# Optimization experiments

Measured on AMD Instinct MI355X. Metric: run time of the kernel, lower is better.

Reference implementation:

```python
import jax, jax.numpy as jnp
import numpy as np

VP, B, C, H, W = 8, 2, 512, 16, 16
N_HEAD = 8


def setup_inputs() -> dict:
    key = jax.random.key(0)
    k0, k1, k2, k3, k4 = jax.random.split(key, 5)
    x = jax.random.normal(k0, (VP, B, C, H, W), dtype=jnp.float32)
    s = 1.0 / np.sqrt(C)
    Wqkv = jax.random.normal(k1, (C, 3 * C), dtype=jnp.float32) * s
    bqkv = jnp.zeros((3 * C,), dtype=jnp.float32)
    Wo = jax.random.normal(k2, (C, C), dtype=jnp.float32) * s
    bo = jnp.zeros((C,), dtype=jnp.float32)
    return {"x": x, "Wqkv": Wqkv, "bqkv": bqkv, "Wo": Wo, "bo": bo}


def reference(x, Wqkv, bqkv, Wo, bo):
    vp, b, c, h, w = x.shape
    hw = h * w
    T = vp * hw
    hd = c // N_HEAD
    # 'v b c h w -> b (v h w) c'
    xs = jnp.transpose(x, (1, 0, 3, 4, 2)).reshape(b, T, c)
    qkv = xs @ Wqkv + bqkv  # [b, T, 3c]
    q, k, v = jnp.split(qkv, 3, axis=-1)
    def heads(t):
        return jnp.transpose(t.reshape(b, T, N_HEAD, hd), (0, 2, 1, 3))  # [b, nh, T, hd]
    q, k, v = heads(q), heads(k), heads(v)
    scale = 1.0 / np.sqrt(hd)
    att = jnp.einsum('bhqd,bhkd->bhqk', q, k) * scale  # [b, nh, T, T]
    # block-causal mask: token in block i attends to all tokens in blocks 0..i
    blk = jnp.arange(T) // hw
    allowed = blk[None, :] <= blk[:, None]  # [T, T]
    att = jnp.where(allowed, att, -jnp.inf)
    att = jax.nn.softmax(att, axis=-1)
    y = jnp.einsum('bhqk,bhkd->bhqd', att, v)  # [b, nh, T, hd]
    y = jnp.transpose(y, (0, 2, 1, 3)).reshape(b, T, c)
    y = y @ Wo + bo
    # 'b (v h w) c -> v b c h w'
    y = jnp.transpose(y.reshape(b, vp, h, w, c), (1, 0, 4, 2, 3))
    return y
```

## Files before the change

kernel.cpp:

```cpp
#include <hip/hip_runtime.h>
#include <hip/hip_bf16.h>
#include <stdint.h>

#define VPn 8
#define BBn 2
#define CCn 512
#define NHn 8
#define HDn 64
#define Tn  2048
#define Mn  4096
#define N1n 1536
#define Kn  512
#define QSC 0.180336880111120425f

typedef __attribute__((ext_vector_type(8))) short bf16x8;
typedef __attribute__((ext_vector_type(4))) short s16x4;
typedef __attribute__((ext_vector_type(4))) float f32x4;
typedef __attribute__((ext_vector_type(16))) float f32x16;
typedef unsigned short u16;
typedef unsigned int   u32;

__device__ __forceinline__ u16 f2bf(float f) {
  return __builtin_bit_cast(u16, __float2bfloat16(f));
}
__device__ __forceinline__ void gload16(const void* g, void* l) {
  __builtin_amdgcn_global_load_lds(
      (const __attribute__((address_space(1))) u32*)g,
      (__attribute__((address_space(3))) u32*)l, 16, 0, 0);
}

__global__ __launch_bounds__(256) void conv_x(const float* __restrict__ x, u16* __restrict__ A) {
  int bi = blockIdx.x;
  int vb = bi >> 5;
  int ct = (bi >> 2) & 7;
  int ht = bi & 3;
  int v = vb >> 1, b = vb & 1;
  __shared__ float t[64][65];
  int tid = threadIdx.x, col = tid & 63, r4 = tid >> 6;
  const float* src = x + ((size_t)vb * CCn + ct * 64) * 256 + ht * 64;
#pragma unroll
  for (int i = 0; i < 16; ++i) {
    int row = i * 4 + r4;
    t[row][col] = src[row * 256 + col];
  }
  __syncthreads();
  u16* dst = A + ((size_t)(b * Tn + v * 256 + ht * 64)) * Kn + ct * 64;
#pragma unroll
  for (int i = 0; i < 16; ++i) {
    int row = i * 4 + r4;
    dst[row * Kn + col] = f2bf(t[col][row]);
  }
}

__global__ __launch_bounds__(256) void convw(const float* __restrict__ Win, u16* __restrict__ Wt,
                                             int R, int Cc) {
  int tpr = Cc >> 6;
  int rt = blockIdx.x / tpr, ct = blockIdx.x % tpr;
  __shared__ float t[64][65];
  int tid = threadIdx.x, col = tid & 63, r4 = tid >> 6;
  const float* src = Win + (size_t)(rt * 64) * Cc + ct * 64;
#pragma unroll
  for (int i = 0; i < 16; ++i) {
    int row = i * 4 + r4;
    t[row][col] = src[row * Cc + col];
  }
  __syncthreads();
  u16* dst = Wt + (size_t)(ct * 64) * R + rt * 64;
#pragma unroll
  for (int i = 0; i < 16; ++i) {
    int row = i * 4 + r4;
    dst[row * R + col] = f2bf(t[col][row]);
  }
}


__global__ __launch_bounds__(256, 2) void gemm_qkv(
    const u16* __restrict__ A, const u16* __restrict__ Bt, const float* __restrict__ bias,
    u16* __restrict__ Qo, u16* __restrict__ Kp, u16* __restrict__ Vp) {
  const int nt = N1n / 128;
  int m0 = (blockIdx.x / nt) * 64;
  int n0 = (blockIdx.x % nt) * 128;
  __shared__ __align__(16) u16 As[64 * 64];
  __shared__ __align__(16) u16 Bs[128 * 64];
  int tid = threadIdx.x, lane = tid & 63, w = tid >> 6;
  int wr = w & 1, wc = w >> 1;
  int li = lane & 15, g = lane >> 4;
  int rsub = lane >> 3, slot = lane & 7;
  int srcslot = slot ^ rsub;
  f32x4 acc[2][4] = {};
  for (int k0 = 0; k0 < Kn; k0 += 64) {
    __syncthreads();
#pragma unroll
    for (int i = 0; i < 2; ++i) {
      int ci = w * 2 + i;
      int row = ci * 8 + rsub;
      gload16(A + (size_t)(m0 + row) * Kn + k0 + srcslot * 8, (char*)As + ci * 1024);
    }
#pragma unroll
    for (int i = 0; i < 4; ++i) {
      int ci = w * 4 + i;
      int row = ci * 8 + rsub;
      gload16(Bt + (size_t)(n0 + row) * Kn + k0 + srcslot * 8, (char*)Bs + ci * 1024);
    }
    __syncthreads();
#pragma unroll
    for (int kk = 0; kk < 2; ++kk) {
      bf16x8 af[2], bfr[4];
#pragma unroll
      for (int mi = 0; mi < 2; ++mi) {
        int row = wr * 32 + mi * 16 + li;
        int sw = ((kk * 4 + g) ^ (row & 7)) * 8;
        af[mi] = *(const bf16x8*)(As + row * 64 + sw);
      }
#pragma unroll
      for (int ni = 0; ni < 4; ++ni) {
        int row = wc * 64 + ni * 16 + li;
        int sw = ((kk * 4 + g) ^ (row & 7)) * 8;
        bfr[ni] = *(const bf16x8*)(Bs + row * 64 + sw);
      }
#pragma unroll
      for (int mi = 0; mi < 2; ++mi)
#pragma unroll
        for (int ni = 0; ni < 4; ++ni)
          acc[mi][ni] = __builtin_amdgcn_mfma_f32_16x16x32_bf16(af[mi], bfr[ni], acc[mi][ni], 0, 0, 0);
    }
  }
#pragma unroll
  for (int ni = 0; ni < 4; ++ni) {
    int n = n0 + wc * 64 + ni * 16 + li;
    float bn = bias[n];
    int sel = n >> 9, c = n & 511, hh = c >> 6, d = c & 63;
    if (sel == 0) {
#pragma unroll
      for (int mi = 0; mi < 2; ++mi) {
#pragma unroll
        for (int r = 0; r < 4; ++r) {
          int m = m0 + wr * 32 + mi * 16 + g * 4 + r;
          int bq = m >> 11, t = m & 2047;
          Qo[((size_t)((bq * NHn + hh) * Tn + t)) * HDn + d] = f2bf((acc[mi][ni][r] + bn) * QSC);
        }
      }
    } else if (sel == 1) {
      int kc = d >> 4, khi = (d >> 3) & 1, kj = d & 7;
#pragma unroll
      for (int mi = 0; mi < 2; ++mi) {
#pragma unroll
        for (int r = 0; r < 4; ++r) {
          int m = m0 + wr * 32 + mi * 16 + g * 4 + r;
          int bq = m >> 11, t = m & 2047;
          size_t off = (size_t)(bq * NHn + hh) * 131072 + (size_t)(t >> 5) * 2048 +
                       kc * 512 + khi * 256 + (t & 31) * 8 + kj;
          Kp[off] = f2bf(acc[mi][ni][r] + bn);
        }
      }
    } else {
      int dh = d >> 5, lqd = d & 31;
#pragma unroll
      for (int mi = 0; mi < 2; ++mi) {
        int mb = m0 + wr * 32 + mi * 16 + g * 4;
        int bq = mb >> 11, t0 = mb & 2047;
        size_t off = (size_t)(bq * NHn + hh) * 131072 + (size_t)(t0 >> 5) * 2048 +
                     dh * 1024 + ((t0 >> 4) & 1) * 512 + lqd * 16 +
                     ((t0 >> 2) & 1) * 8 + ((t0 >> 3) & 1) * 4;
        s16x4 ov;
#pragma unroll
        for (int r = 0; r < 4; ++r) ov[r] = (short)f2bf(acc[mi][ni][r] + bn);
        *(s16x4*)(Vp + off) = ov;
      }
    }
  }
}

__global__ __launch_bounds__(256, 4) void attn(
    const u16* __restrict__ Q, const u16* __restrict__ Kp, const u16* __restrict__ Vp,
    u16* __restrict__ Y) {
  int idx = blockIdx.x;
  int bh = (idx & 7) | (((idx >> 3) & 1) << 3);
  int qt = 63 - (idx >> 4);
  int b = bh >> 3, h = bh & 7;
  int qrow0 = qt << 5;
  int nkeys = ((qt >> 3) + 1) << 8;
  int qtr = nkeys >> 2;
  int tid = threadIdx.x;
  int w = tid >> 6;
  int kbeg = w * qtr, kend = kbeg + qtr;
  int lane = tid & 63;
  int lq = lane & 31;
  int hi = lane >> 5;

  const u16* Qb = Q + ((size_t)(bh * Tn + qrow0)) * HDn;
  const u16* Kb = Kp + (size_t)bh * 131072;
  const u16* Vb = Vp + (size_t)bh * 131072;
  int kof = hi * 256 + lq * 8;
  int vof = lq * 16 + hi * 8;

  bf16x8 qf[4];
  {
    const u16* qp = Qb + (size_t)lq * HDn + hi * 8;
#pragma unroll
    for (int c = 0; c < 4; ++c) qf[c] = *(const bf16x8*)(qp + c * 16);
  }

  float mrun = -1e30f, lrun = 0.f;
  f32x16 oacc0 = {}, oacc1 = {};

  bf16x8 kc[4];
#pragma unroll
  for (int c = 0; c < 4; ++c)
    kc[c] = *(const bf16x8*)(Kb + (size_t)(kbeg >> 5) * 2048 + c * 512 + kof);

  for (int k0 = kbeg; k0 < kend; k0 += 32) {
    int kt = k0 >> 5;
    int ktn = (k0 + 32 < kend) ? (kt + 1) : kt;
    bf16x8 knf[4];
#pragma unroll
    for (int c = 0; c < 4; ++c)
      knf[c] = *(const bf16x8*)(Kb + (size_t)ktn * 2048 + c * 512 + kof);
    const u16* vt = Vb + (size_t)kt * 2048 + vof;
    bf16x8 va0 = *(const bf16x8*)(vt);
    bf16x8 vb0 = *(const bf16x8*)(vt + 512);
    bf16x8 va1 = *(const bf16x8*)(vt + 1024);
    bf16x8 vb1 = *(const bf16x8*)(vt + 1536);

    f32x16 s = {};
    __builtin_amdgcn_s_setprio(1);
#pragma unroll
    for (int c = 0; c < 4; ++c)
      s = __builtin_amdgcn_mfma_f32_32x32x16_bf16(kc[c], qf[c], s, 0, 0, 0);
    __builtin_amdgcn_s_setprio(0);

    float m0 = fmaxf(fmaxf(fmaxf(fmaxf(s[0], s[1]), fmaxf(s[2], s[3])),
                           fmaxf(fmaxf(s[4], s[5]), fmaxf(s[6], s[7]))),
                     fmaxf(fmaxf(fmaxf(s[8], s[9]), fmaxf(s[10], s[11])),
                           fmaxf(fmaxf(s[12], s[13]), fmaxf(s[14], s[15]))));
    float mall = fmaxf(m0, __shfl_xor(m0, 32));
    if (!__all(mall <= mrun + 8.0f)) {
      float mnew = fmaxf(mrun, mall);
      float fc = exp2f(mrun - mnew);
      mrun = mnew;
      lrun *= fc;
#pragma unroll
      for (int j = 0; j < 16; ++j) { oacc0[j] *= fc; oacc1[j] *= fc; }
    }
    float p[16];
#pragma unroll
    for (int j = 0; j < 16; ++j) p[j] = exp2f(s[j] - mrun);
    lrun += (((p[0] + p[1]) + (p[2] + p[3])) + ((p[4] + p[5]) + (p[6] + p[7]))) +
            (((p[8] + p[9]) + (p[10] + p[11])) + ((p[12] + p[13]) + (p[14] + p[15])));

    u32 cw[8];
#pragma unroll
    for (int a = 0; a < 8; ++a)
      cw[a] = (u32)f2bf(p[2 * a]) | ((u32)f2bf(p[2 * a + 1]) << 16);
    bf16x8 pfA, pfB;
    {
      __attribute__((ext_vector_type(4))) int pa = {(int)cw[0], (int)cw[1], (int)cw[2], (int)cw[3]};
      __attribute__((ext_vector_type(4))) int pb = {(int)cw[4], (int)cw[5], (int)cw[6], (int)cw[7]};
      pfA = __builtin_bit_cast(bf16x8, pa);
      pfB = __builtin_bit_cast(bf16x8, pb);
    }

    __builtin_amdgcn_s_setprio(1);
    oacc0 = __builtin_amdgcn_mfma_f32_32x32x16_bf16(va0, pfA, oacc0, 0, 0, 0);
    oacc0 = __builtin_amdgcn_mfma_f32_32x32x16_bf16(vb0, pfB, oacc0, 0, 0, 0);
    oacc1 = __builtin_amdgcn_mfma_f32_32x32x16_bf16(va1, pfA, oacc1, 0, 0, 0);
    oacc1 = __builtin_amdgcn_mfma_f32_32x32x16_bf16(vb1, pfB, oacc1, 0, 0, 0);
    __builtin_amdgcn_s_setprio(0);
#pragma unroll
    for (int c = 0; c < 4; ++c) kc[c] = knf[c];
  }

  lrun += __shfl_xor(lrun, 32);

  __shared__ float Ol[4][32][68];
  __shared__ float ml[2][4][32];
  {
    float* op = &Ol[w][lq][hi * 4];
#pragma unroll
    for (int a = 0; a < 4; ++a) {
      f32x4 v0 = {oacc0[4 * a], oacc0[4 * a + 1], oacc0[4 * a + 2], oacc0[4 * a + 3]};
      f32x4 v1 = {oacc1[4 * a], oacc1[4 * a + 1], oacc1[4 * a + 2], oacc1[4 * a + 3]};
      *(f32x4*)(op + a * 8) = v0;
      *(f32x4*)(op + 32 + a * 8) = v1;
    }
    if (lane < 32) { ml[0][w][lq] = mrun; ml[1][w][lq] = lrun; }
  }
  __syncthreads();

#pragma unroll
  for (int task = tid; task < 512; task += 256) {
    int q = task >> 4, quad = task & 15;
    float m0v = ml[0][0][q], m1v = ml[0][1][q], m2v = ml[0][2][q], m3v = ml[0][3][q];
    float mx = fmaxf(fmaxf(m0v, m1v), fmaxf(m2v, m3v));
    float w0 = exp2f(m0v - mx), w1 = exp2f(m1v - mx);
    float w2 = exp2f(m2v - mx), w3 = exp2f(m3v - mx);
    float l = ml[1][0][q] * w0 + ml[1][1][q] * w1 + ml[1][2][q] * w2 + ml[1][3][q] * w3;
    float inv = 1.0f / l;
    f32x4 o0 = *(const f32x4*)&Ol[0][q][quad * 4];
    f32x4 o1 = *(const f32x4*)&Ol[1][q][quad * 4];
    f32x4 o2 = *(const f32x4*)&Ol[2][q][quad * 4];
    f32x4 o3 = *(const f32x4*)&Ol[3][q][quad * 4];
    s16x4 y;
#pragma unroll
    for (int r = 0; r < 4; ++r)
      y[r] = (short)f2bf((o0[r] * w0 + o1[r] * w1 + o2[r] * w2 + o3[r] * w3) * inv);
    *(s16x4*)(Y + ((size_t)(b * Tn + qrow0 + q)) * CCn + h * HDn + quad * 4) = y;
  }
}

__global__ __launch_bounds__(256, 2) void gemm_out(
    const u16* __restrict__ A, const u16* __restrict__ Bt, const float* __restrict__ bias,
    float* __restrict__ Y2) {
  const int nt = 4;
  int m0 = (blockIdx.x / nt) * 64;
  int n0 = (blockIdx.x % nt) * 128;
  __shared__ __align__(16) u16 As[64 * 64];
  __shared__ __align__(16) u16 Bs[128 * 64];
  int tid = threadIdx.x, lane = tid & 63, w = tid >> 6;
  int wr = w & 1, wc = w >> 1;
  int li = lane & 15, g = lane >> 4;
  int rsub = lane >> 3, slot = lane & 7;
  int srcslot = slot ^ rsub;
  f32x4 acc[2][4] = {};
  for (int k0 = 0; k0 < Kn; k0 += 64) {
    __syncthreads();
#pragma unroll
    for (int i = 0; i < 2; ++i) {
      int ci = w * 2 + i;
      int row = ci * 8 + rsub;
      gload16(A + (size_t)(m0 + row) * Kn + k0 + srcslot * 8, (char*)As + ci * 1024);
    }
#pragma unroll
    for (int i = 0; i < 4; ++i) {
      int ci = w * 4 + i;
      int row = ci * 8 + rsub;
      gload16(Bt + (size_t)(n0 + row) * Kn + k0 + srcslot * 8, (char*)Bs + ci * 1024);
    }
    __syncthreads();
#pragma unroll
    for (int kk = 0; kk < 2; ++kk) {
      bf16x8 af[2], bfr[4];
#pragma unroll
      for (int mi = 0; mi < 2; ++mi) {
        int row = wr * 32 + mi * 16 + li;
        int sw = ((kk * 4 + g) ^ (row & 7)) * 8;
        af[mi] = *(const bf16x8*)(As + row * 64 + sw);
      }
#pragma unroll
      for (int ni = 0; ni < 4; ++ni) {
        int row = wc * 64 + ni * 16 + li;
        int sw = ((kk * 4 + g) ^ (row & 7)) * 8;
        bfr[ni] = *(const bf16x8*)(Bs + row * 64 + sw);
      }
#pragma unroll
      for (int mi = 0; mi < 2; ++mi)
#pragma unroll
        for (int ni = 0; ni < 4; ++ni)
          acc[mi][ni] = __builtin_amdgcn_mfma_f32_16x16x32_bf16(af[mi], bfr[ni], acc[mi][ni], 0, 0, 0);
    }
  }
#pragma unroll
  for (int ni = 0; ni < 4; ++ni) {
    int n = n0 + wc * 64 + ni * 16 + li;
    float bn = bias[n];
#pragma unroll
    for (int mi = 0; mi < 2; ++mi) {
#pragma unroll
      for (int r = 0; r < 4; ++r) {
        int m = m0 + wr * 32 + mi * 16 + g * 4 + r;
        Y2[(size_t)m * CCn + n] = acc[mi][ni][r] + bn;
      }
    }
  }
}

__global__ __launch_bounds__(256) void otrans(const float* __restrict__ Y2, float* __restrict__ out) {
  int bi = blockIdx.x;
  int vb = bi >> 5;
  int ht = (bi >> 3) & 3;
  int ct = bi & 7;
  int v = vb >> 1, b = vb & 1;
  __shared__ float t[64][65];
  int tid = threadIdx.x, col = tid & 63, r4 = tid >> 6;
  const float* src = Y2 + (size_t)(b * Tn + v * 256 + ht * 64) * CCn + ct * 64;
#pragma unroll
  for (int i = 0; i < 16; ++i) {
    int row = i * 4 + r4;
    t[row][col] = src[(size_t)row * CCn + col];
  }
  __syncthreads();
  float* dst = out + ((size_t)vb * CCn + ct * 64) * 256 + ht * 64;
#pragma unroll
  for (int i = 0; i < 16; ++i) {
    int row = i * 4 + r4;
    dst[(size_t)row * 256 + col] = t[col][row];
  }
}

extern "C" void kernel_launch(void* const* d_in, const int* in_sizes, int n_in,
                              void* d_out, int out_size, void* d_ws, size_t ws_size,
                              hipStream_t stream) {
  (void)in_sizes; (void)n_in; (void)out_size; (void)ws_size;
  const float* x    = (const float*)d_in[0];
  const float* Wqkv = (const float*)d_in[1];
  const float* bqkv = (const float*)d_in[2];
  const float* Wo   = (const float*)d_in[3];
  const float* bo   = (const float*)d_in[4];
  float* out = (float*)d_out;
  char* ws = (char*)d_ws;
  const size_t MB = 1ull << 20;
  u16*   Abf   = (u16*)(ws + 0);
  u16*   WqkvT = (u16*)(ws + 4 * MB);
  u16*   WoT   = (u16*)(ws + 5 * MB + 512 * 1024);
  u16*   Qb    = (u16*)(ws + 6 * MB);
  u16*   Kb    = (u16*)(ws + 10 * MB);
  u16*   VTb   = (u16*)(ws + 14 * MB);
  float* Y2    = (float*)(ws + 6 * MB);

  conv_x<<<512, 256, 0, stream>>>(x, Abf);
  convw<<<192, 256, 0, stream>>>(Wqkv, WqkvT, Kn, N1n);
  convw<<<64, 256, 0, stream>>>(Wo, WoT, Kn, CCn);
  gemm_qkv<<<64 * 12, 256, 0, stream>>>(Abf, WqkvT, bqkv, Qb, Kb, VTb);
  attn<<<1024, 256, 0, stream>>>(Qb, Kb, VTb, Abf);
  gemm_out<<<64 * 4, 256, 0, stream>>>(Abf, WoT, bo, Y2);
  otrans<<<512, 256, 0, stream>>>(Y2, out);
}
```

Baseline: 71.90 us.

## Fuse output transpose into out-projection GEMM and use packed bf16 converts

Removes the separate otrans kernel and the Y2 fp32 intermediate by having gemm_out write directly in the v b c h w layout with f32x4 stores along hw. The out GEMM tile shrinks to 64x64 to double the block count, with occupancy raised to 4. The scalar bf16 conversions in the attention P packing, the V store and the Y store are replaced by the v_cvt_pk_bf16_f32 inline asm. The trade-offs are less B-tile reuse per block and strided output stores across channels.

Measured after the change: 62.22 us. 1.16x faster.

```diff
diff --git a/kernel.cpp b/kernel.cpp
--- a/kernel.cpp
+++ b/kernel.cpp
@@ -17,11 +17,17 @@
 typedef __attribute__((ext_vector_type(4))) short s16x4;
 typedef __attribute__((ext_vector_type(4))) float f32x4;
 typedef __attribute__((ext_vector_type(16))) float f32x16;
+typedef __attribute__((ext_vector_type(2))) unsigned int u32x2;
 typedef unsigned short u16;
 typedef unsigned int   u32;
 
 __device__ __forceinline__ u16 f2bf(float f) {
   return __builtin_bit_cast(u16, __float2bfloat16(f));
+}
+__device__ __forceinline__ u32 cvtpk(float lo, float hi) {
+  u32 r;
+  asm("v_cvt_pk_bf16_f32 %0, %1, %2" : "=v"(r) : "v"(lo), "v"(hi));
+  return r;
 }
 __device__ __forceinline__ void gload16(const void* g, void* l) {
   __builtin_amdgcn_global_load_lds(
@@ -162,10 +168,10 @@
         size_t off = (size_t)(bq * NHn + hh) * 131072 + (size_t)(t0 >> 5) * 2048 +
                      dh * 1024 + ((t0 >> 4) & 1) * 512 + lqd * 16 +
                      ((t0 >> 2) & 1) * 8 + ((t0 >> 3) & 1) * 4;
-        s16x4 ov;
-#pragma unroll
-        for (int r = 0; r < 4; ++r) ov[r] = (short)f2bf(acc[mi][ni][r] + bn);
-        *(s16x4*)(Vp + off) = ov;
+        u32x2 ov;
+        ov.x = cvtpk(acc[mi][ni][0] + bn, acc[mi][ni][1] + bn);
+        ov.y = cvtpk(acc[mi][ni][2] + bn, acc[mi][ni][3] + bn);
+        *(u32x2*)(Vp + off) = ov;
       }
     }
   }
@@ -248,14 +254,14 @@
     lrun += (((p[0] + p[1]) + (p[2] + p[3])) + ((p[4] + p[5]) + (p[6] + p[7]))) +
             (((p[8] + p[9]) + (p[10] + p[11])) + ((p[12] + p[13]) + (p[14] + p[15])));
 
-    u32 cw[8];
-#pragma unroll
-    for (int a = 0; a < 8; ++a)
-      cw[a] = (u32)f2bf(p[2 * a]) | ((u32)f2bf(p[2 * a + 1]) << 16);
     bf16x8 pfA, pfB;
     {
-      __attribute__((ext_vector_type(4))) int pa = {(int)cw[0], (int)cw[1], (int)cw[2], (int)cw[3]};
-      __attribute__((ext_vector_type(4))) int pb = {(int)cw[4], (int)cw[5], (int)cw[6], (int)cw[7]};
+      __attribute__((ext_vector_type(4))) int pa = {
+          (int)cvtpk(p[0], p[1]), (int)cvtpk(p[2], p[3]),
+          (int)cvtpk(p[4], p[5]), (int)cvtpk(p[6], p[7])};
+      __attribute__((ext_vector_type(4))) int pb = {
+          (int)cvtpk(p[8], p[9]), (int)cvtpk(p[10], p[11]),
+          (int)cvtpk(p[12], p[13]), (int)cvtpk(p[14], p[15])};
       pfA = __builtin_bit_cast(bf16x8, pa);
       pfB = __builtin_bit_cast(bf16x8, pb);
     }
@@ -300,46 +306,44 @@
     f32x4 o1 = *(const f32x4*)&Ol[1][q][quad * 4];
     f32x4 o2 = *(const f32x4*)&Ol[2][q][quad * 4];
     f32x4 o3 = *(const f32x4*)&Ol[3][q][quad * 4];
-    s16x4 y;
-#pragma unroll
-    for (int r = 0; r < 4; ++r)
-      y[r] = (short)f2bf((o0[r] * w0 + o1[r] * w1 + o2[r] * w2 + o3[r] * w3) * inv);
-    *(s16x4*)(Y + ((size_t)(b * Tn + qrow0 + q)) * CCn + h * HDn + quad * 4) = y;
-  }
-}
-
-__global__ __launch_bounds__(256, 2) void gemm_out(
+    float y0 = (o0[0] * w0 + o1[0] * w1 + o2[0] * w2 + o3[0] * w3) * inv;
+    float y1 = (o0[1] * w0 + o1[1] * w1 + o2[1] * w2 + o3[1] * w3) * inv;
+    float y2 = (o0[2] * w0 + o1[2] * w1 + o2[2] * w2 + o3[2] * w3) * inv;
+    float y3 = (o0[3] * w0 + o1[3] * w1 + o2[3] * w2 + o3[3] * w3) * inv;
+    u32x2 yv;
+    yv.x = cvtpk(y0, y1);
+    yv.y = cvtpk(y2, y3);
+    *(u32x2*)(Y + ((size_t)(b * Tn + qrow0 + q)) * CCn + h * HDn + quad * 4) = yv;
+  }
+}
+
+__global__ __launch_bounds__(256, 4) void gemm_out(
     const u16* __restrict__ A, const u16* __restrict__ Bt, const float* __restrict__ bias,
-    float* __restrict__ Y2) {
-  const int nt = 4;
+    float* __restrict__ out) {
+  const int nt = 8;
   int m0 = (blockIdx.x / nt) * 64;
-  int n0 = (blockIdx.x % nt) * 128;
+  int n0 = (blockIdx.x % nt) * 64;
   __shared__ __align__(16) u16 As[64 * 64];
-  __shared__ __align__(16) u16 Bs[128 * 64];
+  __shared__ __align__(16) u16 Bs[64 * 64];
   int tid = threadIdx.x, lane = tid & 63, w = tid >> 6;
   int wr = w & 1, wc = w >> 1;
   int li = lane & 15, g = lane >> 4;
   int rsub = lane >> 3, slot = lane & 7;
   int srcslot = slot ^ rsub;
-  f32x4 acc[2][4] = {};
+  f32x4 acc[2][2] = {};
   for (int k0 = 0; k0 < Kn; k0 += 64) {
     __syncthreads();
 #pragma unroll
     for (int i = 0; i < 2; ++i) {
       int ci = w * 2 + i;
       int row = ci * 8 + rsub;
-      gload16(A + (size_t)(m0 + row) * Kn + k0 + srcslot * 8, (char*)As + ci * 1024);
-    }
-#pragma unroll
-    for (int i = 0; i < 4; ++i) {
-      int ci = w * 4 + i;
-      int row = ci * 8 + rsub;
+      gload16(A  + (size_t)(m0 + row) * Kn + k0 + srcslot * 8, (char*)As + ci * 1024);
       gload16(Bt + (size_t)(n0 + row) * Kn + k0 + srcslot * 8, (char*)Bs + ci * 1024);
     }
     __syncthreads();
 #pragma unroll
     for (int kk = 0; kk < 2; ++kk) {
-      bf16x8 af[2], bfr[4];
+      bf16x8 af[2], bfr[2];
 #pragma unroll
       for (int mi = 0; mi < 2; ++mi) {
         int row = wr * 32 + mi * 16 + li;
@@ -347,53 +351,32 @@
         af[mi] = *(const bf16x8*)(As + row * 64 + sw);
       }
 #pragma unroll
-      for (int ni = 0; ni < 4; ++ni) {
-        int row = wc * 64 + ni * 16 + li;
+      for (int ni = 0; ni < 2; ++ni) {
+        int row = wc * 32 + ni * 16 + li;
         int sw = ((kk * 4 + g) ^ (row & 7)) * 8;
         bfr[ni] = *(const bf16x8*)(Bs + row * 64 + sw);
       }
 #pragma unroll
       for (int mi = 0; mi < 2; ++mi)
 #pragma unroll
-        for (int ni = 0; ni < 4; ++ni)
+        for (int ni = 0; ni < 2; ++ni)
           acc[mi][ni] = __builtin_amdgcn_mfma_f32_16x16x32_bf16(af[mi], bfr[ni], acc[mi][ni], 0, 0, 0);
     }
   }
-#pragma unroll
-  for (int ni = 0; ni < 4; ++ni) {
-    int n = n0 + wc * 64 + ni * 16 + li;
+  int b = m0 >> 11, v = (m0 >> 8) & 7, hw0 = m0 & 255;
+  float* ob = out + (size_t)((v * 2 + b) * 512) * 256;
+#pragma unroll
+  for (int ni = 0; ni < 2; ++ni) {
+    int n = n0 + wc * 32 + ni * 16 + li;
     float bn = bias[n];
 #pragma unroll
     for (int mi = 0; mi < 2; ++mi) {
-#pragma unroll
-      for (int r = 0; r < 4; ++r) {
-        int m = m0 + wr * 32 + mi * 16 + g * 4 + r;
-        Y2[(size_t)m * CCn + n] = acc[mi][ni][r] + bn;
-      }
-    }
-  }
-}
-
-__global__ __launch_bounds__(256) void otrans(const float* __restrict__ Y2, float* __restrict__ out) {
-  int bi = blockIdx.x;
-  int vb = bi >> 5;
-  int ht = (bi >> 3) & 3;
-  int ct = bi & 7;
-  int v = vb >> 1, b = vb & 1;
-  __shared__ float t[64][65];
-  int tid = threadIdx.x, col = tid & 63, r4 = tid >> 6;
-  const float* src = Y2 + (size_t)(b * Tn + v * 256 + ht * 64) * CCn + ct * 64;
-#pragma unroll
-  for (int i = 0; i < 16; ++i) {
-    int row = i * 4 + r4;
-    t[row][col] = src[(size_t)row * CCn + col];
-  }
-  __syncthreads();
-  float* dst = out + ((size_t)vb * CCn + ct * 64) * 256 + ht * 64;
-#pragma unroll
-  for (int i = 0; i < 16; ++i) {
-    int row = i * 4 + r4;
-    dst[(size_t)row * 256 + col] = t[col][row];
+      int hw = hw0 + wr * 32 + mi * 16 + g * 4;
+      f32x4 y;
+#pragma unroll
+      for (int r = 0; r < 4; ++r) y[r] = acc[mi][ni][r] + bn;
+      *(f32x4*)(ob + (size_t)n * 256 + hw) = y;
+    }
   }
 }
 
@@ -415,13 +398,11 @@
   u16*   Qb    = (u16*)(ws + 6 * MB);
   u16*   Kb    = (u16*)(ws + 10 * MB);
   u16*   VTb   = (u16*)(ws + 14 * MB);
-  float* Y2    = (float*)(ws + 6 * MB);
 
   conv_x<<<512, 256, 0, stream>>>(x, Abf);
   convw<<<192, 256, 0, stream>>>(Wqkv, WqkvT, Kn, N1n);
   convw<<<64, 256, 0, stream>>>(Wo, WoT, Kn, CCn);
   gemm_qkv<<<64 * 12, 256, 0, stream>>>(Abf, WqkvT, bqkv, Qb, Kb, VTb);
   attn<<<1024, 256, 0, stream>>>(Qb, Kb, VTb, Abf);
-  gemm_out<<<64 * 4, 256, 0, stream>>>(Abf, WoT, bo, Y2);
-  otrans<<<512, 256, 0, stream>>>(Y2, out);
-}
+  gemm_out<<<64 * 8, 256, 0, stream>>>(Abf, WoT, bo, out);
+}
```
